# Kernel tuning notes

Hardware: AMD Instinct MI355X
Metric: run time of the kernel (lower is better)

The kernel has to match this reference:

```python
import jax, jax.numpy as jnp
import numpy as np

V, E, H, B, S = 32000, 256, 512, 64, 2048


def lstm_step(x, h, c, w_ih, w_hh, b_ih, b_hh):
    # single-timestep LSTM cell, PyTorch gate order (i, f, g, o)
    g = x @ w_ih.T + h @ w_hh.T + b_ih + b_hh  # [B, 4H]
    i, f, gg, o = jnp.split(g, 4, axis=-1)
    i = jax.nn.sigmoid(i)
    f = jax.nn.sigmoid(f)
    o = jax.nn.sigmoid(o)
    gg = jnp.tanh(gg)
    c2 = f * c + i * gg
    h2 = o * jnp.tanh(c2)
    return h2, c2


def setup_inputs() -> dict:
    key = jax.random.key(0)
    ks = jax.random.split(key, 20)
    sc = 0.02
    return {
        "x": jax.random.randint(ks[0], (B,), 0, V),
        "hidden_state_decoder": jax.random.normal(ks[1], (B, H), jnp.float32),
        "hidden_state_encoder": jax.random.normal(ks[2], (B, S, H), jnp.float32),
        "hidden_state": jax.random.normal(ks[3], (1, B, H), jnp.float32),
        "cell_state": jax.random.normal(ks[4], (1, B, H), jnp.float32),
        "emb": jax.random.normal(ks[5], (V, E), jnp.float32) * sc,
        "w_ih1": jax.random.normal(ks[6], (4 * H, E + H), jnp.float32) * sc,
        "w_hh1": jax.random.normal(ks[7], (4 * H, H), jnp.float32) * sc,
        "b_ih1": jnp.zeros((4 * H,), jnp.float32),
        "b_hh1": jnp.zeros((4 * H,), jnp.float32),
        "w_ih": jax.random.normal(ks[8], (3, 4 * H, H), jnp.float32) * sc,  # lstm2..4
        "w_hh": jax.random.normal(ks[9], (3, 4 * H, H), jnp.float32) * sc,
        "b_ih": jnp.zeros((3, 4 * H), jnp.float32),
        "b_hh": jnp.zeros((3, 4 * H), jnp.float32),
        "fc_w": jax.random.normal(ks[10], (V, H), jnp.float32) * sc,
        "fc_b": jnp.zeros((V,), jnp.float32),
    }


def reference(x, hidden_state_decoder, hidden_state_encoder, hidden_state, cell_state,
              emb, w_ih1, w_hh1, b_ih1, b_hh1, w_ih, w_hh, b_ih, b_hh, fc_w, fc_b):
    # embedding gather: [B, E]
    xe = emb[x]
    # dot-product attention (Luong): scores [B, S]
    scores = jnp.einsum('bd,bsd->bs', hidden_state_decoder, hidden_state_encoder)
    attn = jax.nn.softmax(scores, axis=-1)
    ctx = jnp.einsum('bs,bsd->bd', attn, hidden_state_encoder)  # [B, H]
    inp = jnp.concatenate([xe, ctx], axis=-1)  # [B, E+H]
    # lstm1 with provided initial state
    h, c = lstm_step(inp, hidden_state[0], cell_state[0], w_ih1, w_hh1, b_ih1, b_hh1)
    z = h
    zeros = jnp.zeros_like(h)
    # lstm2..4 with zero initial states (PyTorch default)
    for l in range(3):
        h, c = lstm_step(z, zeros, zeros, w_ih[l], w_hh[l], b_ih[l], b_hh[l])
        z = h
    logits = z @ fc_w.T + fc_b  # [B, V]
    logits = logits[:, None, :]  # [B, 1, V]
    return logits, h[None], c[None]
```

## Files before the change

### kernel.cpp

```cpp
#include <hip/hip_runtime.h>
#include <cstdint>
#include <cstddef>

constexpr int B = 64, S = 2048, H = 512, E = 256, V = 32000;
constexpr int NCHUNK = 32;

using bf16x8 = __attribute__((ext_vector_type(8))) short;
using f32x4  = __attribute__((ext_vector_type(4))) float;

static __device__ __forceinline__ unsigned short f2bf(float f) {
    unsigned u = __float_as_uint(f);
    u = u + 0x7fffu + ((u >> 16) & 1u);
    return (unsigned short)(u >> 16);
}

__global__ __launch_bounds__(256) void attn_part_kernel(
    const float* __restrict__ hd, const float* __restrict__ enc,
    float* __restrict__ m_part, float* __restrict__ l_part,
    float* __restrict__ acc_part)
{
    int b = blockIdx.x >> 3;
    int wave = threadIdx.x >> 6, lane = threadIdx.x & 63;
    int chunk = ((blockIdx.x & 7) << 2) + wave;
    int s0 = chunk * 64;

    const float4* hv = (const float4*)(hd + (size_t)b * H);
    float4 h0 = hv[lane], h1 = hv[64 + lane];
    const float4* ev = (const float4*)(enc + (size_t)b * S * H) + (size_t)s0 * (H / 4);

    float m = -1e30f, l = 0.f;
    float4 a0 = make_float4(0.f, 0.f, 0.f, 0.f);
    float4 a1 = make_float4(0.f, 0.f, 0.f, 0.f);
    float4 e0 = ev[lane], e1 = ev[64 + lane];

    auto process = [&](const float4& pe0, const float4& pe1) {
        float p = pe0.x * h0.x + pe0.y * h0.y + pe0.z * h0.z + pe0.w * h0.w
                + pe1.x * h1.x + pe1.y * h1.y + pe1.z * h1.z + pe1.w * h1.w;
#pragma unroll
        for (int off = 32; off; off >>= 1) p += __shfl_xor(p, off, 64);
        if (p <= m) {
            float w = __expf(p - m);
            l += w;
            a0.x += w * pe0.x; a0.y += w * pe0.y; a0.z += w * pe0.z; a0.w += w * pe0.w;
            a1.x += w * pe1.x; a1.y += w * pe1.y; a1.z += w * pe1.z; a1.w += w * pe1.w;
        } else {
            float sc = __expf(m - p);
            m = p;
            l = l * sc + 1.f;
            a0.x = a0.x * sc + pe0.x; a0.y = a0.y * sc + pe0.y;
            a0.z = a0.z * sc + pe0.z; a0.w = a0.w * sc + pe0.w;
            a1.x = a1.x * sc + pe1.x; a1.y = a1.y * sc + pe1.y;
            a1.z = a1.z * sc + pe1.z; a1.w = a1.w * sc + pe1.w;
        }
    };

    for (int s = 0; s < 63; ++s) {
        const float4* r = ev + (size_t)(s + 1) * (H / 4);
        float4 n0 = r[lane], n1 = r[64 + lane];
        process(e0, e1);
        e0 = n0; e1 = n1;
    }
    process(e0, e1);

    int base = b * NCHUNK + chunk;
    if (lane == 0) { m_part[base] = m; l_part[base] = l; }
    float4* ap = (float4*)(acc_part + (size_t)base * H);
    ap[lane] = a0; ap[64 + lane] = a1;
}

__global__ __launch_bounds__(256) void combine_kernel(
    const float* __restrict__ m_part, const float* __restrict__ l_part,
    const float* __restrict__ acc_part, const int* __restrict__ x,
    const float* __restrict__ emb, const float* __restrict__ h0,
    float* __restrict__ inp_t)
{
    int b = blockIdx.x, t = threadIdx.x;
    float M = -1e30f;
    for (int i = 0; i < NCHUNK; ++i) M = fmaxf(M, m_part[b * NCHUNK + i]);
    float L = 0.f;
    for (int i = 0; i < NCHUNK; ++i)
        L += l_part[b * NCHUNK + i] * __expf(m_part[b * NCHUNK + i] - M);
    float invL = 1.f / L;

    for (int d = t; d < H; d += 256) {
        float s = 0.f;
        for (int i = 0; i < NCHUNK; ++i)
            s += __expf(m_part[b * NCHUNK + i] - M) *
                 acc_part[((size_t)(b * NCHUNK + i)) * H + d];
        inp_t[(E + d) * B + b] = s * invL;
    }
    inp_t[t * B + b] = emb[(size_t)x[b] * E + t];
    for (int d = t; d < H; d += 256)
        inp_t[(E + H + d) * B + b] = h0[b * H + d];
}

__global__ __launch_bounds__(256) void lstm_fused_kernel(
    const float* __restrict__ A1, int lda1, int k1len,
    const float* __restrict__ A2, int lda2, int KT,
    const float* __restrict__ X,
    const float* __restrict__ b_ih, const float* __restrict__ b_hh,
    const float* __restrict__ c_prev,
    float* __restrict__ h_t, float* __restrict__ out_h, float* __restrict__ out_c,
    unsigned short* __restrict__ zbf)
{
    __shared__ float As[4][8][33];
    __shared__ float Xs[4][32][64];
    float (*Ps)[8][64] = (float(*)[8][64])&Xs[0][0][0];

    const int t = threadIdx.x;
    const int j0 = blockIdx.x * 2;
    const int QK = KT >> 2;
    const int nIter = QK >> 5;
    const int kq = t >> 6, r = t & 63, ty = r >> 4, tx = r & 15;

    const int sil = (t >> 3) & 7, skc = t & 7;
    const int sgrow = j0 + (sil & 1) + 512 * (sil >> 1);

    float acc[2][4];
#pragma unroll
    for (int i = 0; i < 2; ++i)
#pragma unroll
        for (int j = 0; j < 4; ++j) acc[i][j] = 0.f;

    for (int it = 0; it < nIter; ++it) {
        {
            int gk = kq * QK + it * 32 + skc * 4;
            const float* src = (gk < k1len)
                ? A1 + (size_t)sgrow * lda1 + gk
                : A2 + (size_t)sgrow * lda2 + (gk - k1len);
            *(float4*)&As[kq][sil][skc * 4] = *(const float4*)src;
        }
#pragma unroll
        for (int q = 0; q < 8; ++q) {
            int p = t + q * 256;
            int kk_all = p >> 4, col = (p & 15) * 4;
            int xkq = kk_all >> 5, kk = kk_all & 31;
            int gk = xkq * QK + it * 32 + kk;
            *(float4*)&Xs[xkq][kk][col] = *(const float4*)&X[(size_t)gk * 64 + col];
        }
        __syncthreads();

#pragma unroll 8
        for (int kk = 0; kk < 32; ++kk) {
            float a0 = As[kq][2 * ty + 0][kk];
            float a1 = As[kq][2 * ty + 1][kk];
            float4 xv = *(const float4*)&Xs[kq][kk][tx * 4];
            float xx[4] = {xv.x, xv.y, xv.z, xv.w};
#pragma unroll
            for (int j = 0; j < 4; ++j) {
                acc[0][j] += a0 * xx[j];
                acc[1][j] += a1 * xx[j];
            }
        }
        __syncthreads();
    }

#pragma unroll
    for (int i = 0; i < 2; ++i)
        *(float4*)&Ps[kq][2 * ty + i][tx * 4] =
            make_float4(acc[i][0], acc[i][1], acc[i][2], acc[i][3]);
    __syncthreads();

    for (int idx = t; idx < 8 * 64; idx += 256) {
        int row = idx >> 6, b = idx & 63;
        Ps[0][row][b] = Ps[0][row][b] + Ps[1][row][b] + Ps[2][row][b] + Ps[3][row][b];
    }
    __syncthreads();

    if (t < 128) {
        int jj = t >> 6, b = t & 63;
        int j = j0 + jj;
        float gi = Ps[0][jj + 0][b] + b_ih[j]        + b_hh[j];
        float gf = Ps[0][jj + 2][b] + b_ih[j + 512]  + b_hh[j + 512];
        float gg = Ps[0][jj + 4][b] + b_ih[j + 1024] + b_hh[j + 1024];
        float go = Ps[0][jj + 6][b] + b_ih[j + 1536] + b_hh[j + 1536];
        float iv = 1.f / (1.f + __expf(-gi));
        float fv = 1.f / (1.f + __expf(-gf));
        float gv = tanhf(gg);
        float ov = 1.f / (1.f + __expf(-go));
        float cp = c_prev ? c_prev[b * H + j] : 0.f;
        float c2 = fv * cp + iv * gv;
        float hv = ov * tanhf(c2);
        h_t[j * B + b] = hv;
        if (out_h) { out_h[b * H + j] = hv; out_c[b * H + j] = c2; }
        if (zbf)   { zbf[(size_t)b * H + j] = f2bf(hv); }
    }
}

__global__ __launch_bounds__(256) void fc_mfma_kernel(
    const float* __restrict__ A, const unsigned short* __restrict__ zbf,
    float* __restrict__ outp, const float* __restrict__ bias)
{
    __shared__ float Wt[2][64][36];

    const int t = threadIdx.x;
    const int wv  = t >> 6;
    const int l   = t & 63;
    const int row = l & 15;
    const int kq  = l >> 4;
    const int rl  = wv * 16 + row;
    const int mblk = blockIdx.x * 64;
    const int m0   = mblk + wv * 16;

    const int st_r = t >> 2, st_c = t & 3;
    const float* Asrc = A + (size_t)(mblk + st_r) * 512 + st_c * 8;

    f32x4 acc[4];
#pragma unroll
    for (int bt = 0; bt < 4; ++bt) acc[bt] = (f32x4){0.f, 0.f, 0.f, 0.f};

    {
        float4 v0 = *(const float4*)(Asrc + 0);
        float4 v1 = *(const float4*)(Asrc + 4);
        *(float4*)&Wt[0][st_r][st_c * 8]     = v0;
        *(float4*)&Wt[0][st_r][st_c * 8 + 4] = v1;
    }
    __syncthreads();

    for (int s = 0; s < 16; ++s) {
        const int buf = s & 1;
        if (s < 15) {
            const float* src = Asrc + (s + 1) * 32;
            float4 v0 = *(const float4*)(src + 0);
            float4 v1 = *(const float4*)(src + 4);
            *(float4*)&Wt[buf ^ 1][st_r][st_c * 8]     = v0;
            *(float4*)&Wt[buf ^ 1][st_r][st_c * 8 + 4] = v1;
        }

        const float* wrow = &Wt[buf][rl][kq * 8];
        float4 wa = *(const float4*)wrow;
        float4 wb = *(const float4*)(wrow + 4);
        float wf[8] = {wa.x, wa.y, wa.z, wa.w, wb.x, wb.y, wb.z, wb.w};

        unsigned hd[4], ld[4];
#pragma unroll
        for (int p = 0; p < 4; ++p) {
            unsigned u0 = __float_as_uint(wf[2 * p]);
            unsigned u1 = __float_as_uint(wf[2 * p + 1]);
            hd[p] = (u0 >> 16) | (u1 & 0xffff0000u);
            float r0 = wf[2 * p]     - __uint_as_float(u0 & 0xffff0000u);
            float r1 = wf[2 * p + 1] - __uint_as_float(u1 & 0xffff0000u);
            ld[p] = (__float_as_uint(r0) >> 16) | (__float_as_uint(r1) & 0xffff0000u);
        }
        union { uint4 u; bf16x8 v; } cvh, cvl;
        cvh.u = make_uint4(hd[0], hd[1], hd[2], hd[3]);
        cvl.u = make_uint4(ld[0], ld[1], ld[2], ld[3]);

        const int kgl = s * 32 + kq * 8;
#pragma unroll
        for (int bt = 0; bt < 4; ++bt) {
            int b = bt * 16 + row;
            bf16x8 zf = *(const bf16x8*)(zbf + (size_t)b * 512 + kgl);
            acc[bt] = __builtin_amdgcn_mfma_f32_16x16x32_bf16(cvh.v, zf, acc[bt], 0, 0, 0);
            acc[bt] = __builtin_amdgcn_mfma_f32_16x16x32_bf16(cvl.v, zf, acc[bt], 0, 0, 0);
        }
        __syncthreads();
    }

    int v0 = m0 + kq * 4;
    float4 bv = *(const float4*)&bias[v0];
#pragma unroll
    for (int bt = 0; bt < 4; ++bt) {
        int b = bt * 16 + row;
        float4 o;
        o.x = acc[bt][0] + bv.x;
        o.y = acc[bt][1] + bv.y;
        o.z = acc[bt][2] + bv.z;
        o.w = acc[bt][3] + bv.w;
        *(float4*)&outp[(size_t)b * V + v0] = o;
    }
}

extern "C" void kernel_launch(void* const* d_in, const int* in_sizes, int n_in,
                              void* d_out, int out_size, void* d_ws, size_t ws_size,
                              hipStream_t stream)
{
    const int*   x     = (const int*)d_in[0];
    const float* hdec  = (const float*)d_in[1];
    const float* enc   = (const float*)d_in[2];
    const float* h0    = (const float*)d_in[3];
    const float* c0    = (const float*)d_in[4];
    const float* emb   = (const float*)d_in[5];
    const float* w_ih1 = (const float*)d_in[6];
    const float* w_hh1 = (const float*)d_in[7];
    const float* b_ih1 = (const float*)d_in[8];
    const float* b_hh1 = (const float*)d_in[9];
    const float* w_ih  = (const float*)d_in[10];
    const float* b_ih  = (const float*)d_in[12];
    const float* b_hh  = (const float*)d_in[13];
    const float* fc_w  = (const float*)d_in[14];
    const float* fc_b  = (const float*)d_in[15];

    float* out = (float*)d_out;
    float* ws  = (float*)d_ws;

    float* m_part   = ws;
    float* l_part   = ws + 2048;
    float* acc_part = ws + 4096;
    float* inp_t    = acc_part + (size_t)B * NCHUNK * H;
    float* zA       = inp_t + 1280 * B;
    float* zB       = zA + H * B;
    unsigned short* zbf = (unsigned short*)(zB + H * B);

    float* out_h = out + (size_t)B * V;
    float* out_c = out_h + (size_t)B * H;

    attn_part_kernel<<<512, 256, 0, stream>>>(hdec, enc, m_part, l_part, acc_part);
    combine_kernel<<<64, 256, 0, stream>>>(m_part, l_part, acc_part, x, emb, h0, inp_t);

    lstm_fused_kernel<<<256, 256, 0, stream>>>(
        w_ih1, 768, 768, w_hh1, 512, 1280, inp_t,
        b_ih1, b_hh1, c0, zA, nullptr, nullptr, nullptr);

    lstm_fused_kernel<<<256, 256, 0, stream>>>(
        w_ih + 0 * (size_t)2048 * H, 512, 512, nullptr, 0, 512, zA,
        b_ih + 0 * 2048, b_hh + 0 * 2048, nullptr, zB, nullptr, nullptr, nullptr);
    lstm_fused_kernel<<<256, 256, 0, stream>>>(
        w_ih + 1 * (size_t)2048 * H, 512, 512, nullptr, 0, 512, zB,
        b_ih + 1 * 2048, b_hh + 1 * 2048, nullptr, zA, nullptr, nullptr, nullptr);
    lstm_fused_kernel<<<256, 256, 0, stream>>>(
        w_ih + 2 * (size_t)2048 * H, 512, 512, nullptr, 0, 512, zA,
        b_ih + 2 * 2048, b_hh + 2 * 2048, nullptr, zB, out_h, out_c, zbf);

    fc_mfma_kernel<<<500, 256, 0, stream>>>(fc_w, zbf, out, fc_b);
}
```

Before: 139.1 us.

## Double grid parallelism across attention, combine, and LSTM kernels

```diff
diff --git a/kernel.cpp b/kernel.cpp
--- a/kernel.cpp
+++ b/kernel.cpp
@@ -3,7 +3,7 @@
 #include <cstddef>
 
 constexpr int B = 64, S = 2048, H = 512, E = 256, V = 32000;
-constexpr int NCHUNK = 32;
+constexpr int NCHUNK = 64;
 
 using bf16x8 = __attribute__((ext_vector_type(8))) short;
 using f32x4  = __attribute__((ext_vector_type(4))) float;
@@ -19,10 +19,10 @@
     float* __restrict__ m_part, float* __restrict__ l_part,
     float* __restrict__ acc_part)
 {
-    int b = blockIdx.x >> 3;
+    int b = blockIdx.x >> 4;
     int wave = threadIdx.x >> 6, lane = threadIdx.x & 63;
-    int chunk = ((blockIdx.x & 7) << 2) + wave;
-    int s0 = chunk * 64;
+    int chunk = ((blockIdx.x & 15) << 2) + wave;
+    int s0 = chunk * 32;
 
     const float4* hv = (const float4*)(hd + (size_t)b * H);
     float4 h0 = hv[lane], h1 = hv[64 + lane];
@@ -54,7 +54,7 @@
         }
     };
 
-    for (int s = 0; s < 63; ++s) {
+    for (int s = 0; s < 31; ++s) {
         const float4* r = ev + (size_t)(s + 1) * (H / 4);
         float4 n0 = r[lane], n1 = r[64 + lane];
         process(e0, e1);
@@ -74,24 +74,28 @@
     const float* __restrict__ emb, const float* __restrict__ h0,
     float* __restrict__ inp_t)
 {
-    int b = blockIdx.x, t = threadIdx.x;
+    const int b = blockIdx.x >> 3, part = blockIdx.x & 7, t = threadIdx.x;
     float M = -1e30f;
     for (int i = 0; i < NCHUNK; ++i) M = fmaxf(M, m_part[b * NCHUNK + i]);
     float L = 0.f;
     for (int i = 0; i < NCHUNK; ++i)
         L += l_part[b * NCHUNK + i] * __expf(m_part[b * NCHUNK + i] - M);
-    float invL = 1.f / L;
-
-    for (int d = t; d < H; d += 256) {
-        float s = 0.f;
-        for (int i = 0; i < NCHUNK; ++i)
-            s += __expf(m_part[b * NCHUNK + i] - M) *
-                 acc_part[((size_t)(b * NCHUNK + i)) * H + d];
-        inp_t[(E + d) * B + b] = s * invL;
-    }
-    inp_t[t * B + b] = emb[(size_t)x[b] * E + t];
-    for (int d = t; d < H; d += 256)
-        inp_t[(E + H + d) * B + b] = h0[b * H + d];
+    const float invL = 1.f / L;
+
+    const int d = part * 64 + (t >> 2), sub = t & 3;
+    float s = 0.f;
+    for (int i = sub; i < NCHUNK; i += 4)
+        s += __expf(m_part[b * NCHUNK + i] - M) *
+             acc_part[((size_t)(b * NCHUNK + i)) * H + d];
+    s += __shfl_xor(s, 1, 64);
+    s += __shfl_xor(s, 2, 64);
+    if (sub == 0) inp_t[(E + d) * B + b] = s * invL;
+
+    if (part == 0) inp_t[t * B + b] = emb[(size_t)x[b] * E + t];
+    if (part == 2 || part == 3) {
+        int d2 = (part - 2) * 256 + t;
+        inp_t[(E + H + d2) * B + b] = h0[b * H + d2];
+    }
 }
 
 __global__ __launch_bounds__(256) void lstm_fused_kernel(
@@ -103,32 +107,28 @@
     float* __restrict__ h_t, float* __restrict__ out_h, float* __restrict__ out_c,
     unsigned short* __restrict__ zbf)
 {
-    __shared__ float As[4][8][33];
+    __shared__ float As[4][4][33];
     __shared__ float Xs[4][32][64];
-    float (*Ps)[8][64] = (float(*)[8][64])&Xs[0][0][0];
+    float (*Ps)[4][64] = (float(*)[4][64])&Xs[0][0][0];
 
     const int t = threadIdx.x;
-    const int j0 = blockIdx.x * 2;
+    const int j = blockIdx.x;
     const int QK = KT >> 2;
     const int nIter = QK >> 5;
     const int kq = t >> 6, r = t & 63, ty = r >> 4, tx = r & 15;
 
-    const int sil = (t >> 3) & 7, skc = t & 7;
-    const int sgrow = j0 + (sil & 1) + 512 * (sil >> 1);
-
-    float acc[2][4];
-#pragma unroll
-    for (int i = 0; i < 2; ++i)
-#pragma unroll
-        for (int j = 0; j < 4; ++j) acc[i][j] = 0.f;
+    const int sg = r >> 3, skc = r & 7;
+    const int sgrow = j + 512 * sg;
+
+    float acc[4] = {0.f, 0.f, 0.f, 0.f};
 
     for (int it = 0; it < nIter; ++it) {
-        {
+        if (r < 32) {
             int gk = kq * QK + it * 32 + skc * 4;
             const float* src = (gk < k1len)
                 ? A1 + (size_t)sgrow * lda1 + gk
                 : A2 + (size_t)sgrow * lda2 + (gk - k1len);
-            *(float4*)&As[kq][sil][skc * 4] = *(const float4*)src;
+            *(float4*)&As[kq][sg][skc * 4] = *(const float4*)src;
         }
 #pragma unroll
         for (int q = 0; q < 8; ++q) {
@@ -142,38 +142,29 @@
 
 #pragma unroll 8
         for (int kk = 0; kk < 32; ++kk) {
-            float a0 = As[kq][2 * ty + 0][kk];
-            float a1 = As[kq][2 * ty + 1][kk];
+            float a = As[kq][ty][kk];
             float4 xv = *(const float4*)&Xs[kq][kk][tx * 4];
-            float xx[4] = {xv.x, xv.y, xv.z, xv.w};
-#pragma unroll
-            for (int j = 0; j < 4; ++j) {
-                acc[0][j] += a0 * xx[j];
-                acc[1][j] += a1 * xx[j];
-            }
+            acc[0] += a * xv.x; acc[1] += a * xv.y;
+            acc[2] += a * xv.z; acc[3] += a * xv.w;
         }
         __syncthreads();
     }
 
-#pragma unroll
-    for (int i = 0; i < 2; ++i)
-        *(float4*)&Ps[kq][2 * ty + i][tx * 4] =
-            make_float4(acc[i][0], acc[i][1], acc[i][2], acc[i][3]);
+    *(float4*)&Ps[kq][ty][tx * 4] = make_float4(acc[0], acc[1], acc[2], acc[3]);
     __syncthreads();
 
-    for (int idx = t; idx < 8 * 64; idx += 256) {
-        int row = idx >> 6, b = idx & 63;
-        Ps[0][row][b] = Ps[0][row][b] + Ps[1][row][b] + Ps[2][row][b] + Ps[3][row][b];
+    {
+        int g = t >> 6, b = t & 63;
+        Ps[0][g][b] = Ps[0][g][b] + Ps[1][g][b] + Ps[2][g][b] + Ps[3][g][b];
     }
     __syncthreads();
 
-    if (t < 128) {
-        int jj = t >> 6, b = t & 63;
-        int j = j0 + jj;
-        float gi = Ps[0][jj + 0][b] + b_ih[j]        + b_hh[j];
-        float gf = Ps[0][jj + 2][b] + b_ih[j + 512]  + b_hh[j + 512];
-        float gg = Ps[0][jj + 4][b] + b_ih[j + 1024] + b_hh[j + 1024];
-        float go = Ps[0][jj + 6][b] + b_ih[j + 1536] + b_hh[j + 1536];
+    if (t < 64) {
+        int b = t;
+        float gi = Ps[0][0][b] + b_ih[j]        + b_hh[j];
+        float gf = Ps[0][1][b] + b_ih[j + 512]  + b_hh[j + 512];
+        float gg = Ps[0][2][b] + b_ih[j + 1024] + b_hh[j + 1024];
+        float go = Ps[0][3][b] + b_ih[j + 1536] + b_hh[j + 1536];
         float iv = 1.f / (1.f + __expf(-gi));
         float fv = 1.f / (1.f + __expf(-gf));
         float gv = tanhf(gg);
@@ -295,8 +286,8 @@
     float* ws  = (float*)d_ws;
 
     float* m_part   = ws;
-    float* l_part   = ws + 2048;
-    float* acc_part = ws + 4096;
+    float* l_part   = ws + 4096;
+    float* acc_part = ws + 8192;
     float* inp_t    = acc_part + (size_t)B * NCHUNK * H;
     float* zA       = inp_t + 1280 * B;
     float* zB       = zA + H * B;
@@ -305,20 +296,20 @@
     float* out_h = out + (size_t)B * V;
     float* out_c = out_h + (size_t)B * H;
 
-    attn_part_kernel<<<512, 256, 0, stream>>>(hdec, enc, m_part, l_part, acc_part);
-    combine_kernel<<<64, 256, 0, stream>>>(m_part, l_part, acc_part, x, emb, h0, inp_t);
-
-    lstm_fused_kernel<<<256, 256, 0, stream>>>(
+    attn_part_kernel<<<1024, 256, 0, stream>>>(hdec, enc, m_part, l_part, acc_part);
+    combine_kernel<<<512, 256, 0, stream>>>(m_part, l_part, acc_part, x, emb, h0, inp_t);
+
+    lstm_fused_kernel<<<512, 256, 0, stream>>>(
         w_ih1, 768, 768, w_hh1, 512, 1280, inp_t,
         b_ih1, b_hh1, c0, zA, nullptr, nullptr, nullptr);
 
-    lstm_fused_kernel<<<256, 256, 0, stream>>>(
+    lstm_fused_kernel<<<512, 256, 0, stream>>>(
         w_ih + 0 * (size_t)2048 * H, 512, 512, nullptr, 0, 512, zA,
         b_ih + 0 * 2048, b_hh + 0 * 2048, nullptr, zB, nullptr, nullptr, nullptr);
-    lstm_fused_kernel<<<256, 256, 0, stream>>>(
+    lstm_fused_kernel<<<512, 256, 0, stream>>>(
         w_ih + 1 * (size_t)2048 * H, 512, 512, nullptr, 0, 512, zB,
         b_ih + 1 * 2048, b_hh + 1 * 2048, nullptr, zA, nullptr, nullptr, nullptr);
-    lstm_fused_kernel<<<256, 256, 0, stream>>>(
+    lstm_fused_kernel<<<512, 256, 0, stream>>>(
         w_ih + 2 * (size_t)2048 * H, 512, 512, nullptr, 0, 512, zA,
         b_ih + 2 * 2048, b_hh + 2 * 2048, nullptr, zB, out_h, out_c, zbf);
 
```

Result: slower. 147.5 us (+6.0%).
